# Performance work log

Measured on AMD Instinct MI355X. Metric: run time of the kernel, lower is better.

## Reference

```python
import jax, jax.numpy as jnp
import numpy as np

D_MODEL = 1024
N_HEADS = 16
N_KV_HEADS = 4
HEAD_DIM = D_MODEL // N_HEADS
NUM_REP = N_HEADS // N_KV_HEADS
B, T = 2, 2048


def setup_inputs() -> dict:
    key = jax.random.key(0)
    ks = jax.random.split(key, 9)
    s = 0.02
    x = jax.random.normal(ks[0], (B, T, D_MODEL), dtype=jnp.float32)
    # causal mask: True = masked (matches torch masked_fill semantics)
    mask = jnp.triu(jnp.ones((T, T), dtype=bool), k=1)[None, None]
    kv_dim = N_KV_HEADS * HEAD_DIM
    return {
        "x": x,
        "mask": mask,
        "Wq": jax.random.normal(ks[1], (D_MODEL, D_MODEL), jnp.float32) * s,
        "bq": jnp.zeros((D_MODEL,), jnp.float32),
        "Wk": jax.random.normal(ks[2], (D_MODEL, kv_dim), jnp.float32) * s,
        "bk": jnp.zeros((kv_dim,), jnp.float32),
        "Wv": jax.random.normal(ks[3], (D_MODEL, kv_dim), jnp.float32) * s,
        "bv": jnp.zeros((kv_dim,), jnp.float32),
        "Wo": jax.random.normal(ks[4], (D_MODEL, D_MODEL), jnp.float32) * s,
        "bo": jnp.zeros((D_MODEL,), jnp.float32),
    }


def reference(x, mask, Wq, bq, Wk, bk, Wv, bv, Wo, bo):
    Bx, Tx, C = x.shape
    # projections
    q = (x @ Wq + bq).reshape(Bx, Tx, N_HEADS, HEAD_DIM).transpose(0, 2, 1, 3)  # (B,H,T,D)
    k = (x @ Wk + bk).reshape(Bx, Tx, N_KV_HEADS, HEAD_DIM)
    v = (x @ Wv + bv).reshape(Bx, Tx, N_KV_HEADS, HEAD_DIM)
    # repeat_kv: expand+reshape == repeat along head axis
    k = jnp.repeat(k, NUM_REP, axis=2).transpose(0, 2, 1, 3)  # (B,H,T,D)
    v = jnp.repeat(v, NUM_REP, axis=2).transpose(0, 2, 1, 3)
    scale = 1.0 / jnp.sqrt(jnp.asarray(HEAD_DIM, x.dtype))
    attn = jnp.einsum('bhtd,bhsd->bhts', q, k) * scale  # (B,H,T,T)
    attn = jnp.where(mask, -jnp.inf, attn)
    attn = jax.nn.softmax(attn, axis=-1)
    out = jnp.einsum('bhts,bhsd->bhtd', attn, v)
    out = out.transpose(0, 2, 1, 3).reshape(Bx, Tx, C)
    return out @ Wo + bo
```

## Files before the change

### kernel.cpp

```cpp
#include <hip/hip_runtime.h>
#include <hip/hip_bf16.h>
#include <cmath>
#include <stdint.h>


typedef __attribute__((ext_vector_type(4))) float f32x4;
typedef __attribute__((ext_vector_type(16))) float f32x16;
typedef __attribute__((ext_vector_type(8))) short s16x8;
typedef __attribute__((ext_vector_type(8))) unsigned short u16x8;

#define MFMA32(a, b, c) __builtin_amdgcn_mfma_f32_32x32x16_bf16(a, b, c, 0, 0, 0)

__device__ __forceinline__ unsigned short f2bf(float f) {
    unsigned int u = __float_as_uint(f);
    u += 0x7FFFu + ((u >> 16) & 1u);
    return (unsigned short)(u >> 16);
}

__device__ __forceinline__ unsigned int pktr(float lo, float hi) {
    return __builtin_amdgcn_perm(__float_as_uint(hi), __float_as_uint(lo), 0x07060302u);
}

__device__ __forceinline__ void async16(void* lds, const void* g) {
    __builtin_amdgcn_global_load_lds(
        (const __attribute__((address_space(1))) unsigned int*)g,
        (__attribute__((address_space(3))) unsigned int*)lds, 16, 0, 0);
}

__global__ __launch_bounds__(256) void prep(
        const float* __restrict__ x,
        const float* __restrict__ Wq, const float* __restrict__ Wk,
        const float* __restrict__ Wv, const float* __restrict__ Wo,
        const float* __restrict__ bq, const float* __restrict__ bk,
        const float* __restrict__ bv,
        unsigned short* __restrict__ xb, unsigned short* __restrict__ Wqkv,
        unsigned short* __restrict__ Wot, float* __restrict__ biasq, float qscale) {
    __shared__ unsigned short sx[128 * 72];
    __shared__ float tile[32][33];
    const int bid = blockIdx.x, tid = threadIdx.x;
    if (bid < 512) {
        const int mt = bid >> 4, kt = bid & 15;
#pragma unroll
        for (int i = 0; i < 8; ++i) {
            const int flat = (i * 256 + tid) * 4;
            const int row = flat >> 6, col = flat & 63;
            f32x4 ld = *reinterpret_cast<const f32x4*>(
                &x[(size_t)(mt * 128 + row) * 1024 + kt * 64 + col]);
            unsigned short* d = &sx[row * 72 + col];
            d[0] = f2bf(ld.x); d[1] = f2bf(ld.y); d[2] = f2bf(ld.z); d[3] = f2bf(ld.w);
        }
        __syncthreads();
#pragma unroll
        for (int j = 0; j < 4; ++j) {
            const int idx = j * 256 + tid;
            const int kb = idx >> 7, m = idx & 127;
            u16x8 v = *reinterpret_cast<const u16x8*>(&sx[m * 72 + kb * 8]);
            *reinterpret_cast<u16x8*>(
                &xb[(size_t)(((mt * 16 + kt) * 8 + kb) * 128 + m) * 8]) = v;
        }
    } else if (bid < 3072) {
        int id = bid - 512;
        const float* W; unsigned short* out; int N, nbase; float scale = 1.0f;
        if (id < 1024)      { W = Wq; out = Wqkv; N = 1024; nbase = 0;    scale = qscale; }
        else if (id < 1280) { W = Wk; out = Wqkv; N = 256;  nbase = 1024; id -= 1024; }
        else if (id < 1536) { W = Wv; out = Wqkv; N = 256;  nbase = 1280; id -= 1280; }
        else                { W = Wo; out = Wot;  N = 1024; nbase = 0;    id -= 1536; }
        const int nb = N >> 5;
        const int n0 = (id % nb) * 32, k0 = (id / nb) * 32;
        const int tx = tid & 31, ty = tid >> 5;
#pragma unroll
        for (int r = 0; r < 4; ++r)
            tile[ty + r * 8][tx] = W[(size_t)(k0 + ty + r * 8) * N + n0 + tx];
        __syncthreads();
        const int k = k0 + tx;
#pragma unroll
        for (int r = 0; r < 4; ++r) {
            const int n = nbase + n0 + ty + r * 8;
            size_t addr = (size_t)((n >> 6) * 16 + (k >> 6)) * 4096
                        + (size_t)((((k >> 3) & 7) * 64 + (n & 63)) * 8 + (k & 7));
            out[addr] = f2bf(tile[tx][ty + r * 8] * scale);
        }
    } else {
        const int i = (bid - 3072) * 256 + tid;
        if (i < 1024) biasq[i] = bq[i] * qscale;
        else if (i < 1280) biasq[i] = bk[i - 1024];
        else biasq[i] = bv[i - 1280];
    }
}

template <int EPI>
__global__ __launch_bounds__(256) void gemm_mn(
        const unsigned short* __restrict__ A, const unsigned short* __restrict__ Bt,
        const float* __restrict__ bias,
        unsigned short* __restrict__ oQ, unsigned short* __restrict__ oK,
        unsigned short* __restrict__ oV, float* __restrict__ oF) {
    __shared__ alignas(16) unsigned short sA[8 * 128 * 8];
    __shared__ alignas(16) unsigned short sB[8 * 64 * 8];
    const int tid = threadIdx.x;
    const int lane = tid & 63, w = tid >> 6;
    const int l31 = lane & 31, grp = lane >> 5;
    const int m0 = blockIdx.y * 128, n0 = blockIdx.x * 64;
    const int wm = w * 32;

    f32x16 acc0 = {}, acc1 = {};

    for (int kt = 0; kt < 16; ++kt) {
        const unsigned short* ab = A + ((size_t)(blockIdx.y * 16 + kt)) * 8192 + (size_t)tid * 8;
        const unsigned short* bb = Bt + ((size_t)(blockIdx.x * 16 + kt)) * 4096 + (size_t)tid * 8;
#pragma unroll
        for (int i = 0; i < 4; ++i)
            async16(&sA[(size_t)(i * 256 + (tid & 192)) * 8], ab + (size_t)i * 2048);
#pragma unroll
        for (int i = 0; i < 2; ++i)
            async16(&sB[(size_t)(i * 256 + (tid & 192)) * 8], bb + (size_t)i * 2048);
        __syncthreads();
#pragma unroll
        for (int kc = 0; kc < 4; ++kc) {
            const int kb = kc * 2 + grp;
            s16x8 a  = *reinterpret_cast<const s16x8*>(&sA[(size_t)(kb * 128 + wm + l31) * 8]);
            s16x8 b0 = *reinterpret_cast<const s16x8*>(&sB[(size_t)(kb * 64 + l31) * 8]);
            s16x8 b1 = *reinterpret_cast<const s16x8*>(&sB[(size_t)(kb * 64 + 32 + l31) * 8]);
            acc0 = MFMA32(a, b0, acc0);
            acc1 = MFMA32(a, b1, acc1);
        }
        __syncthreads();
    }
    const float bv0 = bias[n0 + l31], bv1 = bias[n0 + 32 + l31];
#pragma unroll
    for (int r = 0; r < 16; ++r) {
        const int row = m0 + wm + (r & 3) + 8 * (r >> 2) + 4 * grp;
        const float v0 = acc0[r] + bv0, v1 = acc1[r] + bv1;
        if (EPI == 0) {
            if (n0 < 1024) {
                oQ[(size_t)row * 1024 + n0 + l31] = f2bf(v0);
                oQ[(size_t)row * 1024 + n0 + 32 + l31] = f2bf(v1);
            } else if (n0 < 1280) {
                oK[(size_t)row * 256 + (n0 - 1024) + l31] = f2bf(v0);
                oK[(size_t)row * 256 + (n0 - 1024) + 32 + l31] = f2bf(v1);
            } else {
                oV[(size_t)(n0 - 1280 + l31) * 4096 + row] = f2bf(v0);
                oV[(size_t)(n0 - 1280 + 32 + l31) * 4096 + row] = f2bf(v1);
            }
        } else {
            oF[(size_t)row * 1024 + n0 + l31] = v0;
            oF[(size_t)row * 1024 + n0 + 32 + l31] = v1;
        }
    }
}

__global__ __launch_bounds__(256) void flash_attn(
        const unsigned short* __restrict__ Qb, const unsigned short* __restrict__ Kb,
        const unsigned short* __restrict__ Vt, unsigned short* __restrict__ Ot) {
    __shared__ alignas(16) unsigned short sK[64 * 72];
    __shared__ alignas(16) unsigned short sV[64 * 72];
    const int tid = threadIdx.x;
    const int lane = tid & 63, w = tid >> 6;
    const int ln = lane & 31, grp = lane >> 5;
    const int bh = blockIdx.x;
    const int yq = blockIdx.y;
    const int qt = (yq < 8) ? (15 - yq) : (yq - 8);
    const int b = bh >> 4, h = bh & 15, kvh = h >> 2;
    const int t0 = qt * 128;
    const int qrow_g = t0 + w * 32 + ln;

    const unsigned short* Qrow = Qb + (size_t)(b * 2048 + qrow_g) * 1024 + h * 64;
    s16x8 qf[4];
#pragma unroll
    for (int kk = 0; kk < 4; ++kk)
        qf[kk] = *reinterpret_cast<const s16x8*>(Qrow + kk * 16 + grp * 8);

    const unsigned short* Kbase = Kb + (size_t)(b * 2048) * 256 + kvh * 64;
    const unsigned short* Vbase = Vt + (size_t)(kvh * 64) * 4096 + (size_t)b * 2048;

    const int srow = tid >> 3, sd0 = (tid & 7) * 8;
    u16x8 kreg[2], vreg[2];
#pragma unroll
    for (int i = 0; i < 2; ++i) {
        kreg[i] = *reinterpret_cast<const u16x8*>(Kbase + (size_t)(srow + 32 * i) * 256 + sd0);
        vreg[i] = *reinterpret_cast<const u16x8*>(Vbase + (size_t)(srow + 32 * i) * 4096 + sd0);
    }

    f32x16 o0 = {}, o1 = {};
    float ltot = 0.f;
    const int nchunks = 2 * qt + 2;

    for (int c = 0; c < nchunks; ++c) {
        const int s0 = c * 64;
        __syncthreads();
#pragma unroll
        for (int i = 0; i < 2; ++i) {
            *reinterpret_cast<u16x8*>(&sK[(srow + 32 * i) * 72 + sd0]) = kreg[i];
            *reinterpret_cast<u16x8*>(&sV[(srow + 32 * i) * 72 + sd0]) = vreg[i];
        }
        __syncthreads();
        if (c + 1 < nchunks) {
            const int s1 = s0 + 64;
#pragma unroll
            for (int i = 0; i < 2; ++i) {
                kreg[i] = *reinterpret_cast<const u16x8*>(Kbase + (size_t)(s1 + srow + 32 * i) * 256 + sd0);
                vreg[i] = *reinterpret_cast<const u16x8*>(Vbase + (size_t)(srow + 32 * i) * 4096 + s1 + sd0);
            }
        }
        f32x16 st0 = {}, st1 = {};
#pragma unroll
        for (int kk = 0; kk < 4; ++kk) {
            s16x8 k0 = *reinterpret_cast<const s16x8*>(&sK[ln * 72 + kk * 16 + grp * 8]);
            s16x8 k1 = *reinterpret_cast<const s16x8*>(&sK[(32 + ln) * 72 + kk * 16 + grp * 8]);
            st0 = MFMA32(k0, qf[kk], st0);
            st1 = MFMA32(k1, qf[kk], st1);
        }
        if (s0 + 63 > t0 + w * 32) {
#pragma unroll
            for (int r = 0; r < 16; ++r) {
                const int keyo = s0 + (r & 3) + 8 * (r >> 2) + 4 * grp;
                if (keyo > qrow_g)      st0[r] = -INFINITY;
                if (keyo + 32 > qrow_g) st1[r] = -INFINITY;
            }
        }
        f32x16 p0, p1;
#pragma unroll
        for (int r = 0; r < 16; ++r) {
            p0[r] = __builtin_amdgcn_exp2f(st0[r]);
            p1[r] = __builtin_amdgcn_exp2f(st1[r]);
        }
        float a0 = 0.f, a1 = 0.f, a2 = 0.f, a3 = 0.f;
#pragma unroll
        for (int r = 0; r < 16; r += 2) {
            a0 += p0[r]; a1 += p0[r + 1];
            a2 += p1[r]; a3 += p1[r + 1];
        }
        ltot += (a0 + a1) + (a2 + a3);
#pragma unroll
        for (int kkp = 0; kkp < 4; ++kkp) {
            const f32x16& pm = (kkp < 2) ? p0 : p1;
            const int A4 = 8 * (kkp & 1);
            unsigned int pA0 = pktr(pm[A4 + 0], pm[A4 + 1]);
            unsigned int pA1 = pktr(pm[A4 + 2], pm[A4 + 3]);
            unsigned int pB0 = pktr(pm[A4 + 4], pm[A4 + 5]);
            unsigned int pB1 = pktr(pm[A4 + 6], pm[A4 + 7]);
            unsigned int rA0 = (unsigned int)__shfl_xor((int)pA0, 32, 64);
            unsigned int rA1 = (unsigned int)__shfl_xor((int)pA1, 32, 64);
            unsigned int rB0 = (unsigned int)__shfl_xor((int)pB0, 32, 64);
            unsigned int rB1 = (unsigned int)__shfl_xor((int)pB1, 32, 64);
            union { unsigned int u[4]; s16x8 v; } pf;
            pf.u[0] = grp ? rB0 : pA0;
            pf.u[1] = grp ? rB1 : pA1;
            pf.u[2] = grp ? pB0 : rA0;
            pf.u[3] = grp ? pB1 : rA1;
            s16x8 v0 = *reinterpret_cast<const s16x8*>(&sV[ln * 72 + kkp * 16 + grp * 8]);
            s16x8 v1 = *reinterpret_cast<const s16x8*>(&sV[(32 + ln) * 72 + kkp * 16 + grp * 8]);
            o0 = MFMA32(pf.v, v0, o0);
            o1 = MFMA32(pf.v, v1, o1);
        }
    }

    const float lfull = ltot + __shfl_xor(ltot, 32, 64);
    const float rl = 1.0f / lfull;
    unsigned short* Otb = Ot + (size_t)((b * 16 + qt) * 16 + h) * 8192
                             + (size_t)(ln >> 3) * 1024 + (ln & 7);
#pragma unroll
    for (int r = 0; r < 16; ++r) {
        const int row = (r & 3) + 8 * (r >> 2) + 4 * grp;
        const float rr = __shfl(rl, row, 64);
        const size_t off = (size_t)(w * 32 + row) * 8;
        Otb[off]        = f2bf(o0[r] * rr);
        Otb[off + 4096] = f2bf(o1[r] * rr);
    }
}

extern "C" void kernel_launch(void* const* d_in, const int* in_sizes, int n_in,
                              void* d_out, int out_size, void* d_ws, size_t ws_size,
                              hipStream_t stream) {
    const float* x  = (const float*)d_in[0];
    const float* Wq = (const float*)d_in[2];
    const float* bq = (const float*)d_in[3];
    const float* Wk = (const float*)d_in[4];
    const float* bk = (const float*)d_in[5];
    const float* Wv = (const float*)d_in[6];
    const float* bv = (const float*)d_in[7];
    const float* Wo = (const float*)d_in[8];
    const float* bo = (const float*)d_in[9];
    float* out = (float*)d_out;

    char* ws = (char*)d_ws;
    unsigned short* xb    = (unsigned short*)(ws);
    unsigned short* Wqkv  = (unsigned short*)(ws + (8u  << 20));
    unsigned short* Wot   = (unsigned short*)(ws + (12u << 20));
    float*          biasq = (float*)         (ws + (15u << 20));
    unsigned short* Qb    = (unsigned short*)(ws + (16u << 20));
    unsigned short* Kb    = (unsigned short*)(ws + (24u << 20));
    unsigned short* Vtp   = (unsigned short*)(ws + (26u << 20));
    unsigned short* Otl   = (unsigned short*)(ws + (28u << 20));

    const float qscale = 0.125f * 1.4426950408889634f;

    prep<<<3078, 256, 0, stream>>>(x, Wq, Wk, Wv, Wo, bq, bk, bv,
                                   xb, Wqkv, Wot, biasq, qscale);
    gemm_mn<0><<<dim3(24, 32), 256, 0, stream>>>(xb, Wqkv, biasq, Qb, Kb, Vtp, nullptr);
    flash_attn<<<dim3(32, 16), 256, 0, stream>>>(Qb, Kb, Vtp, Otl);
    gemm_mn<1><<<dim3(16, 32), 256, 0, stream>>>(Otl, Wot, bo, nullptr, nullptr, nullptr, out);
}
```

Baseline: 180.0 us.

## Double-buffer GEMM LDS tiles and pair causal query tiles in attention blocks

The GEMM kernel now double-buffers its LDS A/B tiles, prefetching the next K-slice asynchronously while computing the current one, which drops one barrier per iteration. The flash attention kernel now uses 512-thread blocks that pair a short and a long causal query tile (qp and 15-qp). Both tiles share one streamed K/V buffer, double-buffered in LDS, so load work is balanced and K/V fetches are shared across the pair. The P-matrix exchange also uses two cross-half shuffles instead of four. The cost is more LDS per block, and in attention the short-tile waves idle through the later chunks while the long tile finishes.

```diff
diff --git a/kernel.cpp b/kernel.cpp
--- a/kernel.cpp
+++ b/kernel.cpp
@@ -94,36 +94,48 @@
         const float* __restrict__ bias,
         unsigned short* __restrict__ oQ, unsigned short* __restrict__ oK,
         unsigned short* __restrict__ oV, float* __restrict__ oF) {
-    __shared__ alignas(16) unsigned short sA[8 * 128 * 8];
-    __shared__ alignas(16) unsigned short sB[8 * 64 * 8];
+    __shared__ alignas(16) unsigned short sA[2][8 * 128 * 8];
+    __shared__ alignas(16) unsigned short sB[2][8 * 64 * 8];
     const int tid = threadIdx.x;
     const int lane = tid & 63, w = tid >> 6;
     const int l31 = lane & 31, grp = lane >> 5;
     const int m0 = blockIdx.y * 128, n0 = blockIdx.x * 64;
     const int wm = w * 32;
 
+    const unsigned short* Abase = A + (size_t)blockIdx.y * (16 * 8192) + (size_t)tid * 8;
+    const unsigned short* Bbase = Bt + (size_t)blockIdx.x * (16 * 4096) + (size_t)tid * 8;
+
     f32x16 acc0 = {}, acc1 = {};
 
+#pragma unroll
+    for (int i = 0; i < 4; ++i)
+        async16(&sA[0][(size_t)(i * 256 + (tid & 192)) * 8], Abase + (size_t)i * 2048);
+#pragma unroll
+    for (int i = 0; i < 2; ++i)
+        async16(&sB[0][(size_t)(i * 256 + (tid & 192)) * 8], Bbase + (size_t)i * 2048);
+
     for (int kt = 0; kt < 16; ++kt) {
-        const unsigned short* ab = A + ((size_t)(blockIdx.y * 16 + kt)) * 8192 + (size_t)tid * 8;
-        const unsigned short* bb = Bt + ((size_t)(blockIdx.x * 16 + kt)) * 4096 + (size_t)tid * 8;
-#pragma unroll
-        for (int i = 0; i < 4; ++i)
-            async16(&sA[(size_t)(i * 256 + (tid & 192)) * 8], ab + (size_t)i * 2048);
-#pragma unroll
-        for (int i = 0; i < 2; ++i)
-            async16(&sB[(size_t)(i * 256 + (tid & 192)) * 8], bb + (size_t)i * 2048);
+        const int cur = kt & 1;
         __syncthreads();
+        if (kt < 15) {
+            const unsigned short* ab = Abase + (size_t)(kt + 1) * 8192;
+            const unsigned short* bb = Bbase + (size_t)(kt + 1) * 4096;
+#pragma unroll
+            for (int i = 0; i < 4; ++i)
+                async16(&sA[cur ^ 1][(size_t)(i * 256 + (tid & 192)) * 8], ab + (size_t)i * 2048);
+#pragma unroll
+            for (int i = 0; i < 2; ++i)
+                async16(&sB[cur ^ 1][(size_t)(i * 256 + (tid & 192)) * 8], bb + (size_t)i * 2048);
+        }
 #pragma unroll
         for (int kc = 0; kc < 4; ++kc) {
             const int kb = kc * 2 + grp;
-            s16x8 a  = *reinterpret_cast<const s16x8*>(&sA[(size_t)(kb * 128 + wm + l31) * 8]);
-            s16x8 b0 = *reinterpret_cast<const s16x8*>(&sB[(size_t)(kb * 64 + l31) * 8]);
-            s16x8 b1 = *reinterpret_cast<const s16x8*>(&sB[(size_t)(kb * 64 + 32 + l31) * 8]);
+            s16x8 a  = *reinterpret_cast<const s16x8*>(&sA[cur][(size_t)(kb * 128 + wm + l31) * 8]);
+            s16x8 b0 = *reinterpret_cast<const s16x8*>(&sB[cur][(size_t)(kb * 64 + l31) * 8]);
+            s16x8 b1 = *reinterpret_cast<const s16x8*>(&sB[cur][(size_t)(kb * 64 + 32 + l31) * 8]);
             acc0 = MFMA32(a, b0, acc0);
             acc1 = MFMA32(a, b1, acc1);
         }
-        __syncthreads();
     }
     const float bv0 = bias[n0 + l31], bv1 = bias[n0 + 32 + l31];
 #pragma unroll
@@ -148,20 +160,22 @@
     }
 }
 
-__global__ __launch_bounds__(256) void flash_attn(
+__global__ __launch_bounds__(512) void flash_attn(
         const unsigned short* __restrict__ Qb, const unsigned short* __restrict__ Kb,
         const unsigned short* __restrict__ Vt, unsigned short* __restrict__ Ot) {
-    __shared__ alignas(16) unsigned short sK[64 * 72];
-    __shared__ alignas(16) unsigned short sV[64 * 72];
+    __shared__ alignas(16) unsigned short sK[2][64 * 72];
+    __shared__ alignas(16) unsigned short sV[2][64 * 72];
     const int tid = threadIdx.x;
     const int lane = tid & 63, w = tid >> 6;
     const int ln = lane & 31, grp = lane >> 5;
     const int bh = blockIdx.x;
-    const int yq = blockIdx.y;
-    const int qt = (yq < 8) ? (15 - yq) : (yq - 8);
+    const int qp = blockIdx.y;
     const int b = bh >> 4, h = bh & 15, kvh = h >> 2;
-    const int t0 = qt * 128;
-    const int qrow_g = t0 + w * 32 + ln;
+    const int myqt = (w < 4) ? qp : (15 - qp);
+    const int nch_mine = 2 * myqt + 2;
+    const int nch_all = 32 - 2 * qp;
+    const int t0w = myqt * 128 + (w & 3) * 32;
+    const int qrow_g = t0w + ln;
 
     const unsigned short* Qrow = Qb + (size_t)(b * 2048 + qrow_g) * 1024 + h * 64;
     s16x8 qf[4];
@@ -173,96 +187,86 @@
     const unsigned short* Vbase = Vt + (size_t)(kvh * 64) * 4096 + (size_t)b * 2048;
 
     const int srow = tid >> 3, sd0 = (tid & 7) * 8;
-    u16x8 kreg[2], vreg[2];
-#pragma unroll
-    for (int i = 0; i < 2; ++i) {
-        kreg[i] = *reinterpret_cast<const u16x8*>(Kbase + (size_t)(srow + 32 * i) * 256 + sd0);
-        vreg[i] = *reinterpret_cast<const u16x8*>(Vbase + (size_t)(srow + 32 * i) * 4096 + sd0);
-    }
+    u16x8 kreg = *reinterpret_cast<const u16x8*>(Kbase + (size_t)srow * 256 + sd0);
+    u16x8 vreg = *reinterpret_cast<const u16x8*>(Vbase + (size_t)srow * 4096 + sd0);
 
     f32x16 o0 = {}, o1 = {};
     float ltot = 0.f;
-    const int nchunks = 2 * qt + 2;
-
-    for (int c = 0; c < nchunks; ++c) {
-        const int s0 = c * 64;
+
+    for (int c = 0; c < nch_all; ++c) {
+        unsigned short* bK = sK[c & 1];
+        unsigned short* bV = sV[c & 1];
+        *reinterpret_cast<u16x8*>(&bK[srow * 72 + sd0]) = kreg;
+        *reinterpret_cast<u16x8*>(&bV[srow * 72 + sd0]) = vreg;
         __syncthreads();
-#pragma unroll
-        for (int i = 0; i < 2; ++i) {
-            *reinterpret_cast<u16x8*>(&sK[(srow + 32 * i) * 72 + sd0]) = kreg[i];
-            *reinterpret_cast<u16x8*>(&sV[(srow + 32 * i) * 72 + sd0]) = vreg[i];
-        }
-        __syncthreads();
-        if (c + 1 < nchunks) {
-            const int s1 = s0 + 64;
-#pragma unroll
-            for (int i = 0; i < 2; ++i) {
-                kreg[i] = *reinterpret_cast<const u16x8*>(Kbase + (size_t)(s1 + srow + 32 * i) * 256 + sd0);
-                vreg[i] = *reinterpret_cast<const u16x8*>(Vbase + (size_t)(srow + 32 * i) * 4096 + s1 + sd0);
-            }
-        }
-        f32x16 st0 = {}, st1 = {};
-#pragma unroll
-        for (int kk = 0; kk < 4; ++kk) {
-            s16x8 k0 = *reinterpret_cast<const s16x8*>(&sK[ln * 72 + kk * 16 + grp * 8]);
-            s16x8 k1 = *reinterpret_cast<const s16x8*>(&sK[(32 + ln) * 72 + kk * 16 + grp * 8]);
-            st0 = MFMA32(k0, qf[kk], st0);
-            st1 = MFMA32(k1, qf[kk], st1);
-        }
-        if (s0 + 63 > t0 + w * 32) {
+        if (c + 1 < nch_all) {
+            const int s1 = (c + 1) * 64;
+            kreg = *reinterpret_cast<const u16x8*>(Kbase + (size_t)(s1 + srow) * 256 + sd0);
+            vreg = *reinterpret_cast<const u16x8*>(Vbase + (size_t)srow * 4096 + s1 + sd0);
+        }
+        if (c < nch_mine) {
+            const int s0 = c * 64;
+            f32x16 st0 = {}, st1 = {};
+#pragma unroll
+            for (int kk = 0; kk < 4; ++kk) {
+                s16x8 k0 = *reinterpret_cast<const s16x8*>(&bK[ln * 72 + kk * 16 + grp * 8]);
+                s16x8 k1 = *reinterpret_cast<const s16x8*>(&bK[(32 + ln) * 72 + kk * 16 + grp * 8]);
+                st0 = MFMA32(k0, qf[kk], st0);
+                st1 = MFMA32(k1, qf[kk], st1);
+            }
+            if (s0 + 63 > t0w) {
+#pragma unroll
+                for (int r = 0; r < 16; ++r) {
+                    const int keyo = s0 + (r & 3) + 8 * (r >> 2) + 4 * grp;
+                    if (keyo > qrow_g)      st0[r] = -INFINITY;
+                    if (keyo + 32 > qrow_g) st1[r] = -INFINITY;
+                }
+            }
+            f32x16 p0, p1;
 #pragma unroll
             for (int r = 0; r < 16; ++r) {
-                const int keyo = s0 + (r & 3) + 8 * (r >> 2) + 4 * grp;
-                if (keyo > qrow_g)      st0[r] = -INFINITY;
-                if (keyo + 32 > qrow_g) st1[r] = -INFINITY;
-            }
-        }
-        f32x16 p0, p1;
-#pragma unroll
-        for (int r = 0; r < 16; ++r) {
-            p0[r] = __builtin_amdgcn_exp2f(st0[r]);
-            p1[r] = __builtin_amdgcn_exp2f(st1[r]);
-        }
-        float a0 = 0.f, a1 = 0.f, a2 = 0.f, a3 = 0.f;
-#pragma unroll
-        for (int r = 0; r < 16; r += 2) {
-            a0 += p0[r]; a1 += p0[r + 1];
-            a2 += p1[r]; a3 += p1[r + 1];
-        }
-        ltot += (a0 + a1) + (a2 + a3);
-#pragma unroll
-        for (int kkp = 0; kkp < 4; ++kkp) {
-            const f32x16& pm = (kkp < 2) ? p0 : p1;
-            const int A4 = 8 * (kkp & 1);
-            unsigned int pA0 = pktr(pm[A4 + 0], pm[A4 + 1]);
-            unsigned int pA1 = pktr(pm[A4 + 2], pm[A4 + 3]);
-            unsigned int pB0 = pktr(pm[A4 + 4], pm[A4 + 5]);
-            unsigned int pB1 = pktr(pm[A4 + 6], pm[A4 + 7]);
-            unsigned int rA0 = (unsigned int)__shfl_xor((int)pA0, 32, 64);
-            unsigned int rA1 = (unsigned int)__shfl_xor((int)pA1, 32, 64);
-            unsigned int rB0 = (unsigned int)__shfl_xor((int)pB0, 32, 64);
-            unsigned int rB1 = (unsigned int)__shfl_xor((int)pB1, 32, 64);
-            union { unsigned int u[4]; s16x8 v; } pf;
-            pf.u[0] = grp ? rB0 : pA0;
-            pf.u[1] = grp ? rB1 : pA1;
-            pf.u[2] = grp ? pB0 : rA0;
-            pf.u[3] = grp ? pB1 : rA1;
-            s16x8 v0 = *reinterpret_cast<const s16x8*>(&sV[ln * 72 + kkp * 16 + grp * 8]);
-            s16x8 v1 = *reinterpret_cast<const s16x8*>(&sV[(32 + ln) * 72 + kkp * 16 + grp * 8]);
-            o0 = MFMA32(pf.v, v0, o0);
-            o1 = MFMA32(pf.v, v1, o1);
+                p0[r] = __builtin_amdgcn_exp2f(st0[r]);
+                p1[r] = __builtin_amdgcn_exp2f(st1[r]);
+            }
+            float a0 = 0.f, a1 = 0.f, a2 = 0.f, a3 = 0.f;
+#pragma unroll
+            for (int r = 0; r < 16; r += 2) {
+                a0 += p0[r]; a1 += p0[r + 1];
+                a2 += p1[r]; a3 += p1[r + 1];
+            }
+            ltot += (a0 + a1) + (a2 + a3);
+#pragma unroll
+            for (int kkp = 0; kkp < 4; ++kkp) {
+                const f32x16& pm = (kkp < 2) ? p0 : p1;
+                const int A4 = 8 * (kkp & 1);
+                unsigned int pA0 = pktr(pm[A4 + 0], pm[A4 + 1]);
+                unsigned int pA1 = pktr(pm[A4 + 2], pm[A4 + 3]);
+                unsigned int pB0 = pktr(pm[A4 + 4], pm[A4 + 5]);
+                unsigned int pB1 = pktr(pm[A4 + 6], pm[A4 + 7]);
+                unsigned int x0 = (unsigned int)__shfl_xor((int)(grp ? pA0 : pB0), 32, 64);
+                unsigned int x1 = (unsigned int)__shfl_xor((int)(grp ? pA1 : pB1), 32, 64);
+                union { unsigned int u[4]; s16x8 v; } pf;
+                pf.u[0] = grp ? x0 : pA0;
+                pf.u[1] = grp ? x1 : pA1;
+                pf.u[2] = grp ? pB0 : x0;
+                pf.u[3] = grp ? pB1 : x1;
+                s16x8 v0 = *reinterpret_cast<const s16x8*>(&bV[ln * 72 + kkp * 16 + grp * 8]);
+                s16x8 v1 = *reinterpret_cast<const s16x8*>(&bV[(32 + ln) * 72 + kkp * 16 + grp * 8]);
+                o0 = MFMA32(pf.v, v0, o0);
+                o1 = MFMA32(pf.v, v1, o1);
+            }
         }
     }
 
     const float lfull = ltot + __shfl_xor(ltot, 32, 64);
     const float rl = 1.0f / lfull;
-    unsigned short* Otb = Ot + (size_t)((b * 16 + qt) * 16 + h) * 8192
+    unsigned short* Otb = Ot + (size_t)((b * 16 + myqt) * 16 + h) * 8192
                              + (size_t)(ln >> 3) * 1024 + (ln & 7);
 #pragma unroll
     for (int r = 0; r < 16; ++r) {
         const int row = (r & 3) + 8 * (r >> 2) + 4 * grp;
         const float rr = __shfl(rl, row, 64);
-        const size_t off = (size_t)(w * 32 + row) * 8;
+        const size_t off = (size_t)((w & 3) * 32 + row) * 8;
         Otb[off]        = f2bf(o0[r] * rr);
         Otb[off + 4096] = f2bf(o1[r] * rr);
     }
@@ -297,6 +301,6 @@
     prep<<<3078, 256, 0, stream>>>(x, Wq, Wk, Wv, Wo, bq, bk, bv,
                                    xb, Wqkv, Wot, biasq, qscale);
     gemm_mn<0><<<dim3(24, 32), 256, 0, stream>>>(xb, Wqkv, biasq, Qb, Kb, Vtp, nullptr);
-    flash_attn<<<dim3(32, 16), 256, 0, stream>>>(Qb, Kb, Vtp, Otl);
+    flash_attn<<<dim3(32, 8), 512, 0, stream>>>(Qb, Kb, Vtp, Otl);
     gemm_mn<1><<<dim3(16, 32), 256, 0, stream>>>(Otl, Wot, bo, nullptr, nullptr, nullptr, out);
 }
```

Result: faster. 174.2 us (-3.3%).
